# Kernel tuning notes

Hardware: AMD Instinct MI355X
Metric: run time of the kernel (lower is better)

The kernel has to match this reference:

```python
import jax, jax.numpy as jnp
import numpy as np


def setup_inputs() -> dict:
    key = jax.random.key(0)
    kA, kB = jax.random.split(key)
    N = 8192
    A = jax.random.normal(kA, (N, N), dtype=jnp.float32)
    B = jax.random.normal(kB, (N, N), dtype=jnp.float32)
    return {"A": A, "B": B}


def reference(A, B):
    # Kernel computes C[i,j] = sum_{k=i..j} A[i,k] * B[k,j] for i <= j, 0 elsewhere.
    # This equals triu(triu(A) @ triu(B)): k>=i is enforced by triu(A),
    # k<=j by triu(B), and output restricted to the upper triangle.
    C = jnp.triu(A) @ jnp.triu(B)
    return jnp.triu(C)
```

## Files before the change

### kernel.cpp

```cpp
#include <hip/hip_runtime.h>
#include <hip/hip_bf16.h>
#include <stdint.h>

static constexpr int ND = 8192;

typedef __attribute__((ext_vector_type(8))) short bf16x8;
typedef __attribute__((ext_vector_type(4))) float f32x4;

#define GLOBAL_AS __attribute__((address_space(1)))
#define LDS_AS __attribute__((address_space(3)))

__device__ __forceinline__ void gld_lds16(const void* g, void* l) {
    __builtin_amdgcn_global_load_lds((const GLOBAL_AS void*)g, (LDS_AS void*)l, 16, 0, 0);
}

__device__ __forceinline__ unsigned short f2bf(float x) {
    union { float f; uint32_t u; } v; v.f = x;
    uint32_t u = v.u;
    uint32_t r = (u + 0x7fffu + ((u >> 16) & 1u)) >> 16;
    return (unsigned short)r;
}

__global__ void conv_a(const float* __restrict__ A, unsigned short* __restrict__ Aw) {
    uint32_t g = blockIdx.x * 256u + threadIdx.x;
    int i  = (int)(g >> 10);
    int k0 = (int)(g & 1023u) << 3;
    if (k0 + 8 <= (i & ~255)) return;
    const float* src = A + (size_t)i * ND + k0;
    float4 lo = *(const float4*)src;
    float4 hi = *(const float4*)(src + 4);
    float vals[8] = {lo.x, lo.y, lo.z, lo.w, hi.x, hi.y, hi.z, hi.w};
    unsigned short out[8];
#pragma unroll
    for (int e = 0; e < 8; ++e) {
        int k = k0 + e;
        out[e] = (k >= i) ? f2bf(vals[e]) : (unsigned short)0;
    }
    *(uint4*)(Aw + (size_t)i * ND + k0) = *(const uint4*)out;
}

__global__ void conv_bt(const float* __restrict__ B, unsigned short* __restrict__ Bt) {
    __shared__ float tile[64][65];
    int tk = blockIdx.x, tj = blockIdx.y;
    int t = threadIdx.x;
    int k0 = tk * 64, j0 = tj * 64;

    if (k0 > j0 + 63) {
        if (tk >= ((tj >> 2) + 1) * 4) return;
        int jl = t >> 4;
        int kl = (t & 15) * 4;
#pragma unroll
        for (int r = 0; r < 4; ++r) {
            int j = j0 + jl + r * 16;
            *(uint2*)(Bt + (size_t)j * ND + k0 + kl) = make_uint2(0u, 0u);
        }
        return;
    }
    {
        int kl  = t >> 4;
        int jl4 = (t & 15) * 4;
#pragma unroll
        for (int r = 0; r < 4; ++r) {
            int k = k0 + kl + r * 16;
            float4 v = *(const float4*)(B + (size_t)k * ND + j0 + jl4);
            tile[kl + r * 16][jl4 + 0] = v.x;
            tile[kl + r * 16][jl4 + 1] = v.y;
            tile[kl + r * 16][jl4 + 2] = v.z;
            tile[kl + r * 16][jl4 + 3] = v.w;
        }
    }
    __syncthreads();
    {
        int jl  = t >> 4;
        int kl4 = (t & 15) * 4;
#pragma unroll
        for (int r = 0; r < 4; ++r) {
            int j = j0 + jl + r * 16;
            unsigned short o[4];
#pragma unroll
            for (int e = 0; e < 4; ++e) {
                int k = k0 + kl4 + e;
                float v = tile[kl4 + e][jl + r * 16];
                o[e] = (k <= j) ? f2bf(v) : (unsigned short)0;
            }
            *(uint2*)(Bt + (size_t)j * ND + k0 + kl4) = *(const uint2*)o;
        }
    }
}

__global__ __launch_bounds__(256) void zero_lower(float* __restrict__ C) {
    int bid = blockIdx.x;
    int ti = (int)((1.0f + sqrtf(8.0f * (float)bid + 1.0f)) * 0.5f);
    while (ti * (ti + 1) / 2 <= bid) ++ti;
    while (ti * (ti - 1) / 2 > bid) --ti;
    int tj = bid - ti * (ti - 1) / 2;
    if ((ti >> 1) == (tj >> 1)) return;
    int t = threadIdx.x;
    float* base = C + (size_t)(ti * 128) * ND + tj * 128;
    float4 z = {0.f, 0.f, 0.f, 0.f};
#pragma unroll
    for (int it = 0; it < 16; ++it) {
        int row = it * 8 + (t >> 5);
        *(float4*)(base + (size_t)row * ND + (t & 31) * 4) = z;
    }
}

__global__ __launch_bounds__(256) void zero_split(float* __restrict__ C) {
    int bid = blockIdx.x;
    int tile = bid >> 2, quad = bid & 3;
    int d = 31, rem = tile;
    while (rem >= 32 - d) { rem -= 32 - d; --d; }
    int tib = rem, tjb = tib + d;
    int t = threadIdx.x;
    float* base = C + (size_t)(tib * 256 + (quad >> 1) * 128) * ND
                    + tjb * 256 + (quad & 1) * 128;
    float4 z = {0.f, 0.f, 0.f, 0.f};
#pragma unroll
    for (int it = 0; it < 16; ++it) {
        int row = it * 8 + (t >> 5);
        *(float4*)(base + (size_t)row * ND + (t & 31) * 4) = z;
    }
}

#define BAR() __builtin_amdgcn_s_barrier()
#define WAIT_LGKM0() asm volatile("s_waitcnt lgkmcnt(0)" ::: "memory")
#define WAIT_VM4() asm volatile("s_waitcnt vmcnt(4)" ::: "memory")
#define WAIT_VM0() asm volatile("s_waitcnt vmcnt(0)" ::: "memory")
#define PRIO(x) __builtin_amdgcn_s_setprio(x)

#define LDA(BUF, MH) do { \
    _Pragma("unroll") for (int m_ = 0; m_ < 4; ++m_) \
    _Pragma("unroll") for (int kk_ = 0; kk_ < 2; ++kk_) \
        a_frag[m_][kk_] = *(const bf16x8*)(lds0 + (((BUF)*2 + 0)*2 + (MH))*8192 \
            + (a_lr + m_*16)*64 + (((kk_*4 + khi) ^ lanelo) << 3)); \
} while (0)

#define LDB(BUF, NH) do { \
    _Pragma("unroll") for (int n_ = 0; n_ < 2; ++n_) \
    _Pragma("unroll") for (int kk_ = 0; kk_ < 2; ++kk_) \
        b_frag[NH][n_][kk_] = *(const bf16x8*)(lds0 + (((BUF)*2 + 1)*2 + (NH))*8192 \
            + (b_lr + n_*16)*64 + (((kk_*4 + khi) ^ lanelo) << 3)); \
} while (0)

#define MM(MH, NH) do { \
    _Pragma("unroll") for (int kk_ = 0; kk_ < 2; ++kk_) \
    _Pragma("unroll") for (int m_ = 0; m_ < 4; ++m_) \
    _Pragma("unroll") for (int n_ = 0; n_ < 2; ++n_) \
        acc[(MH)*4 + m_][(NH)*2 + n_] = __builtin_amdgcn_mfma_f32_16x16x32_bf16( \
            a_frag[m_][kk_], b_frag[NH][n_][kk_], acc[(MH)*4 + m_][(NH)*2 + n_], 0, 0, 0); \
} while (0)

__device__ __forceinline__ bool job_map(int bid, int& tib, int& tjb, int& kt0,
                                        int& nkt, bool& atom) {
    static const int cols[8][5] = {
        {31, 16,  8,  4,  0}, {30, 17,  9,  6, -1},
        {29, 18, 10,  7, -1}, {28, 19, 11,  5, -1},
        {27, 20, 12,  3,  1}, {26, 21, 13,  2, -1},
        {25, 22, 14, -1, -1}, {24, 23, 15, -1, -1}};
    int xcd = bid & 7, slot = bid >> 3;
#pragma unroll
    for (int c = 0; c < 5; ++c) {
        int tj = cols[xcd][c];
        if (tj < 0) return false;
        int nsp = (tj - 15 > 0) ? (tj - 15) : 0;
        int n = (tj + 1) + nsp;
        if (slot < n) {
            tjb = tj;
            if (slot < 2 * nsp) {
                tib = slot >> 1;
                nkt = 2 * (tj - tib + 1);
                kt0 = (slot & 1) * nkt;
                atom = true;
            } else {
                tib = nsp + (slot - 2 * nsp);
                nkt = 4 * (tj - tib + 1);
                kt0 = 0;
                atom = false;
            }
            return true;
        }
        slot -= n;
    }
    return false;
}

__global__ __launch_bounds__(512, 2) void gemm_tri8(const unsigned short* __restrict__ Aw,
                                                    const unsigned short* __restrict__ Bt,
                                                    float* __restrict__ C) {
    int tib, tjb, kt0j, nkt;
    bool atom;
    if (!job_map(blockIdx.x, tib, tjb, kt0j, nkt, atom)) return;

    __shared__ __align__(16) unsigned short lds[2][2][2][128][64];
    unsigned short* lds0 = &lds[0][0][0][0][0];

    int t = threadIdx.x;
    int lane = t & 63, w = t >> 6;
    int wr = w >> 2, wc = w & 3;
    int lanelo = lane & 7, khi = lane >> 4;
    int a_lr = wr * 64 + (lane & 15);
    int b_lr = wc * 32 + (lane & 15);

    int kstart = tib * 256 + kt0j * 64;
    int nit = nkt >> 1;

    int srow = w * 8 + (lane >> 3);
    int sg = ((lane & 7) ^ (lane >> 3)) * 8;
    const unsigned short* gA = Aw + (size_t)(tib * 256 + srow) * ND + sg;
    const unsigned short* gB = Bt + (size_t)(tjb * 256 + srow) * ND + sg;
    unsigned short* sdst = lds0 + (w * 512 + lane * 8);

    auto STAGE = [&](int ab, int buf, int h, int ktg) {
        const unsigned short* g = (ab ? gB : gA) + (size_t)(h * 128) * ND + (kstart + ktg * 64);
        unsigned short* l = sdst + ((buf * 2 + ab) * 2 + h) * 8192;
        gld_lds16(g, l);
        gld_lds16(g + (size_t)64 * ND, l + 4096);
    };

    f32x4 acc[8][4];
#pragma unroll
    for (int m = 0; m < 8; ++m)
#pragma unroll
        for (int n = 0; n < 4; ++n) acc[m][n] = (f32x4){0.f, 0.f, 0.f, 0.f};

    bf16x8 a_frag[4][2];
    bf16x8 b_frag[2][2][2];

    STAGE(0, 0, 0, 0); STAGE(1, 0, 0, 0); STAGE(0, 0, 1, 0); STAGE(1, 0, 1, 0);
    STAGE(0, 1, 0, 1); STAGE(1, 1, 0, 1);
    WAIT_VM4();
    BAR();

    for (int I = 0; I < nit; ++I) {
        int k1 = 2 * I + 1, k2 = 2 * I + 2, k3 = 2 * I + 3;
        bool s23 = (k2 < nkt);

        LDA(0, 0); LDB(0, 0);
        STAGE(0, 1, 1, k1);
        BAR(); WAIT_LGKM0(); PRIO(1); MM(0, 0); PRIO(0); BAR();
        LDB(0, 1);
        STAGE(1, 1, 1, k1);
        BAR(); WAIT_LGKM0(); PRIO(1); MM(0, 1); PRIO(0); BAR();
        LDA(0, 1);
        if (s23) STAGE(0, 0, 0, k2);
        BAR(); WAIT_LGKM0(); PRIO(1); MM(1, 0); PRIO(0); BAR();
        if (s23) STAGE(1, 0, 0, k2);
        BAR(); PRIO(1); MM(1, 1); PRIO(0);
        if (s23) { WAIT_VM4(); } else { WAIT_VM0(); }
        BAR();
        LDA(1, 0); LDB(1, 0);
        if (s23) STAGE(0, 0, 1, k2);
        BAR(); WAIT_LGKM0(); PRIO(1); MM(0, 0); PRIO(0); BAR();
        LDB(1, 1);
        if (s23) STAGE(1, 0, 1, k2);
        BAR(); WAIT_LGKM0(); PRIO(1); MM(0, 1); PRIO(0); BAR();
        LDA(1, 1);
        if (s23) STAGE(0, 1, 0, k3);
        BAR(); WAIT_LGKM0(); PRIO(1); MM(1, 0); PRIO(0); BAR();
        if (s23) STAGE(1, 1, 0, k3);
        BAR(); PRIO(1); MM(1, 1); PRIO(0); WAIT_VM4(); BAR();
    }

#pragma unroll
    for (int mh = 0; mh < 2; ++mh)
#pragma unroll
        for (int m = 0; m < 4; ++m)
#pragma unroll
            for (int nh = 0; nh < 2; ++nh)
#pragma unroll
                for (int n = 0; n < 2; ++n) {
                    f32x4 v = acc[mh * 4 + m][nh * 2 + n];
                    int row0 = tib * 256 + mh * 128 + wr * 64 + m * 16 + (lane >> 4) * 4;
                    int col  = tjb * 256 + nh * 128 + wc * 32 + n * 16 + (lane & 15);
                    if (atom) {
#pragma unroll
                        for (int e = 0; e < 4; ++e)
                            atomicAdd(&C[(size_t)(row0 + e) * ND + col], v[e]);
                    } else {
#pragma unroll
                        for (int e = 0; e < 4; ++e)
                            C[(size_t)(row0 + e) * ND + col] = v[e];
                    }
                }
}

__global__ void tri_naive(const float* __restrict__ A, const float* __restrict__ B,
                          float* __restrict__ C) {
    int j = blockIdx.x * 64 + (threadIdx.x & 63);
    int i = blockIdx.y * 4 + (threadIdx.x >> 6);
    float s = 0.f;
    if (j >= i) {
        for (int k = i; k <= j; ++k) s += A[(size_t)i * ND + k] * B[(size_t)k * ND + j];
        C[(size_t)i * ND + j] = s;
    } else {
        C[(size_t)i * ND + j] = 0.f;
    }
}

extern "C" void kernel_launch(void* const* d_in, const int* in_sizes, int n_in,
                              void* d_out, int out_size, void* d_ws, size_t ws_size,
                              hipStream_t stream) {
    (void)in_sizes; (void)n_in; (void)out_size;
    const float* A = (const float*)d_in[0];
    const float* B = (const float*)d_in[1];
    float* C = (float*)d_out;

    const size_t halfws = (size_t)ND * ND * sizeof(unsigned short);
    if (ws_size >= 2 * halfws) {
        unsigned short* Aw = (unsigned short*)d_ws;
        unsigned short* Bt = (unsigned short*)((char*)d_ws + halfws);

        conv_a<<<dim3(ND * (ND / 8) / 256), dim3(256), 0, stream>>>(A, Aw);
        conv_bt<<<dim3(ND / 64, ND / 64), dim3(256), 0, stream>>>(B, Bt);
        zero_lower<<<dim3(2016), dim3(256), 0, stream>>>(C);
        zero_split<<<dim3(544), dim3(256), 0, stream>>>(C);
        gemm_tri8<<<dim3(680), dim3(512), 0, stream>>>(Aw, Bt, C);
    } else {
        tri_naive<<<dim3(ND / 64, ND / 4), dim3(256), 0, stream>>>(A, B, C);
    }
}
```

Measured before the change: 372.1 us.

## Reorder triangular GEMM jobs row-major and split only the longest tiles

Replaces the XCD-aware column table job map with a row-major enumeration over output tile rows. Only the 36 tiles with the longest K range (rows 0-7, far columns) are split in two with atomic accumulation, instead of the 272 split tiles before. The zero_split and gemm grids shrink to match. This cuts atomic traffic and the pre-zeroing it needs, but gives up the explicit per-XCD L2 locality and may leave the load less balanced across CUs.

```diff
diff --git a/kernel.cpp b/kernel.cpp
--- a/kernel.cpp
+++ b/kernel.cpp
@@ -108,11 +108,11 @@
 __global__ __launch_bounds__(256) void zero_split(float* __restrict__ C) {
     int bid = blockIdx.x;
     int tile = bid >> 2, quad = bid & 3;
-    int d = 31, rem = tile;
-    while (rem >= 32 - d) { rem -= 32 - d; --d; }
-    int tib = rem, tjb = tib + d;
+    int ti = 0, rem = tile;
+    while (rem >= 8 - ti) { rem -= 8 - ti; ++ti; }
+    int tjb = 31 - rem;
     int t = threadIdx.x;
-    float* base = C + (size_t)(tib * 256 + (quad >> 1) * 128) * ND
+    float* base = C + (size_t)(ti * 256 + (quad >> 1) * 128) * ND
                     + tjb * 256 + (quad & 1) * 128;
     float4 z = {0.f, 0.f, 0.f, 0.f};
 #pragma unroll
@@ -150,38 +150,31 @@
             a_frag[m_][kk_], b_frag[NH][n_][kk_], acc[(MH)*4 + m_][(NH)*2 + n_], 0, 0, 0); \
 } while (0)
 
-__device__ __forceinline__ bool job_map(int bid, int& tib, int& tjb, int& kt0,
+__device__ __forceinline__ void job_map(int bid, int& tib, int& tjb, int& kt0,
                                         int& nkt, bool& atom) {
-    static const int cols[8][5] = {
-        {31, 16,  8,  4,  0}, {30, 17,  9,  6, -1},
-        {29, 18, 10,  7, -1}, {28, 19, 11,  5, -1},
-        {27, 20, 12,  3,  1}, {26, 21, 13,  2, -1},
-        {25, 22, 14, -1, -1}, {24, 23, 15, -1, -1}};
-    int xcd = bid & 7, slot = bid >> 3;
-#pragma unroll
-    for (int c = 0; c < 5; ++c) {
-        int tj = cols[xcd][c];
-        if (tj < 0) return false;
-        int nsp = (tj - 15 > 0) ? (tj - 15) : 0;
-        int n = (tj + 1) + nsp;
-        if (slot < n) {
-            tjb = tj;
-            if (slot < 2 * nsp) {
-                tib = slot >> 1;
-                nkt = 2 * (tj - tib + 1);
-                kt0 = (slot & 1) * nkt;
+    int ti = 0, rem = bid;
+    for (;;) {
+        int ns = (ti < 8) ? (8 - ti) : 0;
+        int nj = (32 - ti) + ns;
+        if (rem < nj) {
+            tib = ti;
+            if (rem < 2 * ns) {
+                tjb = 31 - (rem >> 1);
+                nkt = 2 * (tjb - ti + 1);
+                kt0 = (rem & 1) * nkt;
                 atom = true;
             } else {
-                tib = nsp + (slot - 2 * nsp);
-                nkt = 4 * (tj - tib + 1);
+                int v = rem - 2 * ns;
+                tjb = 31 - ns - v;
+                nkt = 4 * (tjb - ti + 1);
                 kt0 = 0;
                 atom = false;
             }
-            return true;
+            return;
         }
-        slot -= n;
-    }
-    return false;
+        rem -= nj;
+        ++ti;
+    }
 }
 
 __global__ __launch_bounds__(512, 2) void gemm_tri8(const unsigned short* __restrict__ Aw,
@@ -189,7 +182,7 @@
                                                     float* __restrict__ C) {
     int tib, tjb, kt0j, nkt;
     bool atom;
-    if (!job_map(blockIdx.x, tib, tjb, kt0j, nkt, atom)) return;
+    job_map(blockIdx.x, tib, tjb, kt0j, nkt, atom);
 
     __shared__ __align__(16) unsigned short lds[2][2][2][128][64];
     unsigned short* lds0 = &lds[0][0][0][0][0];
@@ -313,8 +306,8 @@
         conv_a<<<dim3(ND * (ND / 8) / 256), dim3(256), 0, stream>>>(A, Aw);
         conv_bt<<<dim3(ND / 64, ND / 64), dim3(256), 0, stream>>>(B, Bt);
         zero_lower<<<dim3(2016), dim3(256), 0, stream>>>(C);
-        zero_split<<<dim3(544), dim3(256), 0, stream>>>(C);
-        gemm_tri8<<<dim3(680), dim3(512), 0, stream>>>(Aw, Bt, C);
+        zero_split<<<dim3(144), dim3(256), 0, stream>>>(C);
+        gemm_tri8<<<dim3(564), dim3(512), 0, stream>>>(Aw, Bt, C);
     } else {
         tri_naive<<<dim3(ND / 64, ND / 4), dim3(256), 0, stream>>>(A, B, C);
     }
```

Result: faster. 358.5 us (-3.6%).
